# Kernel optimization log

Hardware: AMD Instinct MI355X
Metric: run time of the kernel (lower is better)

The kernel has to match this reference:

```python
import jax, jax.numpy as jnp
import numpy as np

B, S, N, IN_DIM = 64, 12, 170, 1
E, L, C, H, OUT = 128, 4, 2, 8, 1
OFFSET, PAD = 0, 1          # seq_offset=0 -> Conv2d padding (0,1)
LOOKUP, MAXLEN = 0, 100
EPS = 1e-5


def _shift(x, s):
    """y[:, i] = x[:, i+s] along axis 1, zero padded."""
    if s == 0:
        return x
    z = jnp.zeros_like(x[:, :abs(s)])
    if s > 0:
        return jnp.concatenate([x[:, s:], z], axis=1)
    return jnp.concatenate([z, x[:, :s]], axis=1)


def _masked_conv_diag(x, w):
    """Diagonal of Conv2d(kernel=(1,3), pad=(0,PAD)) applied to the causally
    masked repeated tensor, computed directly without the O(B*S*S*E) blowup:
      out[b,i] = sum_k W[:,:,k] @ (mask(i, i+k-PAD) * x[b, i+k-PAD])
    where mask(i,j) = (j <= i) or (j < OFFSET)."""
    i = jnp.arange(x.shape[1])
    out = None
    for k in range(3):
        s = k - PAD
        term = jnp.einsum('bse,oe->bso', _shift(x, s), w[:, :, k])
        if s > 0:  # only future taps can be masked out
            term = term * (i + s < OFFSET).astype(x.dtype)[None, :, None]
        out = term if out is None else out + term
    return out


def _conv1d_k3(x, w, b):
    """Conv1d over the seq dim, kernel 3, padding 1, with bias. x:[b,s,e]."""
    out = b
    for k in range(3):
        out = out + jnp.einsum('bse,oe->bso', _shift(x, k - 1), w[:, :, k])
    return out


def _layer_norm(x, g, b):
    m = jnp.mean(x, -1, keepdims=True)
    v = jnp.mean((x - m) ** 2, -1, keepdims=True)
    return (x - m) * jax.lax.rsqrt(v + EPS) * g + b


def _mha(q_in, kv_in, w, b, mask=None):
    dh = E // H
    q = (q_in @ w[0] + b[0]).reshape(q_in.shape[0], q_in.shape[1], H, dh)
    k = (kv_in @ w[1] + b[1]).reshape(kv_in.shape[0], kv_in.shape[1], H, dh)
    v = (kv_in @ w[2] + b[2]).reshape(kv_in.shape[0], kv_in.shape[1], H, dh)
    s = jnp.einsum('bqhd,bkhd->bhqk', q, k) * np.float32(1.0 / np.sqrt(dh))
    if mask is not None:
        s = jnp.where(mask[None, None], s, jnp.float32(-1e9))
    a = jax.nn.softmax(s, axis=-1)
    o = jnp.einsum('bhqk,bkhd->bqhd', a, v).reshape(q_in.shape[0], q_in.shape[1], E)
    return o @ w[3] + b[3]


def setup_inputs() -> dict:
    key = jax.random.key(0)
    ks = jax.random.split(key, 16)

    def nrm(k, shape, scale=0.05):
        return scale * jax.random.normal(k, shape, dtype=jnp.float32)

    # sinusoidal positional table, length MAXLEN
    pos = np.arange(MAXLEN)[:, None].astype(np.float32)
    div = np.exp(-np.log(10000.0) * np.arange(0, E, 2) / E).astype(np.float32)
    pe = np.zeros((MAXLEN, E), np.float32)
    pe[:, 0::2] = np.sin(pos * div)
    pe[:, 1::2] = np.cos(pos * div)

    return {
        'x': jax.random.normal(ks[0], (B, S, N, IN_DIM), jnp.float32),
        'enc_x': jax.random.normal(ks[1], (C, B * N, S, E), jnp.float32),
        'tgt_mask': jnp.tril(jnp.ones((S, S), bool)),
        'emb_w': nrm(ks[2], (IN_DIM, E), 1.0),
        'emb_b': jnp.zeros((E,), jnp.float32),
        'pe': jnp.asarray(pe),
        'conv_q_w': nrm(ks[3], (L, E, E, 3)),
        'conv_k_w': nrm(ks[4], (L, C, E, E, 3)),
        'conv_k_b': jnp.zeros((L, C, E), jnp.float32),
        'sa_w': nrm(ks[5], (L, 4, E, E)),
        'sa_b': jnp.zeros((L, 4, E), jnp.float32),
        'ca_w': nrm(ks[6], (L, C, 4, E, E)),
        'ca_b': jnp.zeros((L, C, 4, E), jnp.float32),
        'ff_w1': nrm(ks[7], (L, E, 4 * E)),
        'ff_b1': jnp.zeros((L, 4 * E), jnp.float32),
        'ff_w2': nrm(ks[8], (L, 4 * E, E)),
        'ff_b2': jnp.zeros((L, E), jnp.float32),
        'ln_g': jnp.ones((L, 3, E), jnp.float32),
        'ln_b': jnp.zeros((L, 3, E), jnp.float32),
        'fc_w': nrm(ks[9], (E, OUT)),
        'fc_b': jnp.zeros((OUT,), jnp.float32),
    }


def reference(x, enc_x, tgt_mask, emb_w, emb_b, pe, conv_q_w, conv_k_w, conv_k_b,
              sa_w, sa_b, ca_w, ca_b, ff_w1, ff_b1, ff_w2, ff_b2, ln_g, ln_b,
              fc_w, fc_b):
    h = x @ emb_w + emb_b                                    # [B,S,N,E]
    h = jnp.transpose(h, (1, 0, 2, 3)).reshape(S, B * N, E)  # [S,B*N,E]
    h = jnp.transpose(h, (1, 0, 2))                          # [B*N,S,E]
    h = h + pe[LOOKUP:LOOKUP + S]
    for l in range(L):
        # local trends: causal masked-conv query (the fused diagonal)
        h = _masked_conv_diag(h, conv_q_w[l])
        enc_list = [_conv1d_k3(enc_x[i], conv_k_w[l, i], conv_k_b[l, i])
                    for i in range(C)]
        # decoder block: self-attn -> cross-attn (avg over features) -> FFN
        h = _layer_norm(h + _mha(h, h, sa_w[l], sa_b[l], tgt_mask),
                        ln_g[l, 0], ln_b[l, 0])
        cross = sum(_mha(h, enc_list[i], ca_w[l, i], ca_b[l, i])
                    for i in range(C)) / C
        h = _layer_norm(h + cross, ln_g[l, 1], ln_b[l, 1])
        f = jax.nn.relu(h @ ff_w1[l] + ff_b1[l]) @ ff_w2[l] + ff_b2[l]
        h = _layer_norm(h + f, ln_g[l, 2], ln_b[l, 2])
    out = h @ fc_w + fc_b                                    # [B*N,S,OUT]
    out = jnp.transpose(out, (1, 0, 2)).reshape(S, B, N, OUT)
    return jnp.transpose(out, (1, 0, 2, 3))                  # [B,S,N,OUT]
```

## Files before the change

kernel.cpp:

```cpp
#include <hip/hip_runtime.h>


#define B_   64
#define S_   12
#define N_   170
#define BN_  (B_*N_)
#define E_   128
#define L_   4
#define C_   2
#define H_   8
#define DH_  16
#define FF_  512
#define EPS_ 1e-5f
#define THREADS 512

typedef unsigned short u16;
typedef __attribute__((ext_vector_type(4))) float f32x4;
typedef __attribute__((ext_vector_type(8))) u16   us8;
typedef __attribute__((ext_vector_type(4))) u16   us4;
typedef __attribute__((ext_vector_type(8))) __bf16 bf16x8;
union FragU { us8 u; bf16x8 b; };

__device__ __forceinline__ u16 f2bf(float f) {
    __bf16 h = (__bf16)f;
    return __builtin_bit_cast(u16, h);
}
__device__ __forceinline__ float bf2f(u16 s) {
    return __builtin_bit_cast(float, (unsigned)s << 16);
}

__global__ void k_wpack(const float* __restrict__ cq, const float* __restrict__ sa,
                        const float* __restrict__ ck, const float* __restrict__ ca,
                        const float* __restrict__ f1, const float* __restrict__ f2,
                        u16* __restrict__ wp) {
    int f  = blockIdx.x * 256 + threadIdx.x;
    int l  = f / 57344, fl = f % 57344;
    const float* src; int sk, so, KS, q;
    if (fl < 4096)        { int tap = fl >> 11; q = fl & 2047; KS = 4;
                            src = cq + (size_t)l*49152 + tap;            sk = 3;   so = 384; }
    else if (fl < 12288)  { int j = (fl - 4096) >> 11; q = fl & 2047; KS = 4;
                            src = sa + (size_t)(l*4 + j)*16384;          sk = 128; so = 1;   }
    else if (fl < 24576)  { int ct = (fl - 12288) >> 11; q = fl & 2047; KS = 4;
                            int ci = ct / 3, tap = ct % 3;
                            src = ck + (size_t)(l*2 + ci)*49152 + tap;   sk = 3;   so = 384; }
    else if (fl < 40960)  { int cj = (fl - 24576) >> 11; q = fl & 2047; KS = 4;
                            src = ca + (size_t)(l*8 + cj)*16384;         sk = 128; so = 1;   }
    else if (fl < 49152)  { q = fl - 40960; KS = 4;
                            src = f1 + (size_t)l*65536;                  sk = 512; so = 1;   }
    else                  { q = fl - 49152; KS = 16;
                            src = f2 + (size_t)l*65536;                  sk = 128; so = 1;   }
    int lane = q & 63, tt = q >> 6;
    int ks = tt % KS, ntile = tt / KS;
    int k0 = ks*32 + ((lane >> 4) << 3);
    int o  = ntile*16 + (lane & 15);
    us8 w;
    #pragma unroll
    for (int i = 0; i < 8; i++) w[i] = f2bf(src[(size_t)(k0 + i)*sk + (size_t)o*so]);
    *(us8*)(wp + (size_t)f*8) = w;
}

__device__ __forceinline__ void stage48(const float* __restrict__ src, u16* dst, int t) {
    for (int i = t; i < 1536; i += THREADS) {
        const f32x4 v = ((const f32x4*)src)[i];
        int elem = i << 2;
        int row = elem >> 7, colb = (elem & 127) << 1;
        us4 w; w[0] = f2bf(v[0]); w[1] = f2bf(v[1]); w[2] = f2bf(v[2]); w[3] = f2bf(v[3]);
        *(us4*)((char*)dst + (((row << 8) + colb) ^ ((row & 7) << 4))) = w;
    }
}

__device__ __forceinline__ void stage48_embed(const float* __restrict__ x,
    const float* __restrict__ ew, const float* __restrict__ eb,
    const float* __restrict__ pe, int bn0, u16* dst, int t) {
    for (int i = t; i < 1536; i += THREADS) {
        int elem = i << 2;
        int row = elem >> 7, col = elem & 127;
        int g = row / 12, s = row - g*12;
        int bn = bn0 + g, b = bn / N_, n = bn - b*N_;
        float xv = x[(b*S_ + s)*N_ + n];
        const f32x4 w  = *(const f32x4*)(ew + col);
        const f32x4 bb = *(const f32x4*)(eb + col);
        const f32x4 p  = *(const f32x4*)(pe + s*E_ + col);
        us4 o; o[0] = f2bf(xv*w[0] + bb[0] + p[0]); o[1] = f2bf(xv*w[1] + bb[1] + p[1]);
               o[2] = f2bf(xv*w[2] + bb[2] + p[2]); o[3] = f2bf(xv*w[3] + bb[3] + p[3]);
        *(us4*)((char*)dst + (((row << 8) + (col << 1)) ^ ((row & 7) << 4))) = o;
    }
}

__device__ __forceinline__ void acc_init(f32x4 (&acc)[3], const float* bias, int wave, int lane) {
    float bv = bias ? bias[wave*16 + (lane & 15)] : 0.f;
    #pragma unroll
    for (int mt = 0; mt < 3; mt++) {
        acc[mt][0] = bv; acc[mt][1] = bv; acc[mt][2] = bv; acc[mt][3] = bv;
    }
}

template<int KSTOT>
__device__ __forceinline__ void gemm48(const u16* A, const us8* __restrict__ WP, int ksOff,
                                       f32x4 (&acc)[3], int wave, int lane) {
    #pragma unroll
    for (int ks = 0; ks < 4; ks++) {
        bf16x8 a[3];
        #pragma unroll
        for (int mt = 0; mt < 3; mt++) {
            int row  = mt*16 + (lane & 15);
            int colb = (ks*32 + ((lane >> 4) << 3)) << 1;
            FragU fu; fu.u = *(const us8*)((const char*)A + (((row << 8) + colb) ^ ((row & 7) << 4)));
            a[mt] = fu.b;
        }
        FragU fb; fb.u = WP[(wave*KSTOT + ksOff + ks)*64 + lane];
        #pragma unroll
        for (int mt = 0; mt < 3; mt++)
            acc[mt] = __builtin_amdgcn_mfma_f32_16x16x32_bf16(a[mt], fb.b, acc[mt], 0, 0, 0);
    }
}

__device__ __forceinline__ void gemm48_rows(const u16* A, const u16* ZR, const int (&sr)[3],
                                            const us8* __restrict__ WP,
                                            f32x4 (&acc)[3], int wave, int lane) {
    #pragma unroll
    for (int ks = 0; ks < 4; ks++) {
        bf16x8 a[3];
        #pragma unroll
        for (int mt = 0; mt < 3; mt++) {
            int colb = (ks*32 + ((lane >> 4) << 3)) << 1;
            const char* p = (sr[mt] >= 0)
                ? (const char*)A + (((sr[mt] << 8) + colb) ^ ((sr[mt] & 7) << 4))
                : (const char*)ZR + colb;
            FragU fu; fu.u = *(const us8*)p;
            a[mt] = fu.b;
        }
        FragU fb; fb.u = WP[(wave*4 + ks)*64 + lane];
        #pragma unroll
        for (int mt = 0; mt < 3; mt++)
            acc[mt] = __builtin_amdgcn_mfma_f32_16x16x32_bf16(a[mt], fb.b, acc[mt], 0, 0, 0);
    }
}

template<bool RELU>
__device__ __forceinline__ void acc_store_bf(const f32x4 (&acc)[3], u16* Bp, int wave, int lane) {
    #pragma unroll
    for (int mt = 0; mt < 3; mt++)
    #pragma unroll
    for (int r = 0; r < 4; r++) {
        int row = mt*16 + ((lane >> 4) << 2) + r;
        int col = wave*16 + (lane & 15);
        float v = acc[mt][r];
        if (RELU) v = fmaxf(v, 0.f);
        *(u16*)((char*)Bp + (((row << 8) + (col << 1)) ^ ((row & 7) << 4))) = f2bf(v);
    }
}

__device__ __forceinline__ void ld16(const u16* Bf, int row, int colb, float* o16) {
    int x = (row & 7) << 4;
    int base = (row << 8) + colb;
    us8 u0 = *(const us8*)((const char*)Bf + (base ^ x));
    us8 u1 = *(const us8*)((const char*)Bf + ((base + 16) ^ x));
    #pragma unroll
    for (int d = 0; d < 8; d++) { o16[d] = bf2f(u0[d]); o16[8+d] = bf2f(u1[d]); }
}

template<bool MASK>
__device__ __forceinline__ void attn48(u16* QA, const u16* KB, const u16* VB, int t) {
    if (t < 384) {
        int g = t / 96, rem = t % 96;
        int hh = rem / 12, qi = rem % 12;
        int hb2 = hh << 5;
        int rq = g*12 + qi;
        float qv[16]; ld16(QA, rq, hb2, qv);
        float sc[12]; float mx = -1e30f;
        #pragma unroll
        for (int j = 0; j < 12; j++) {
            float kv[16]; ld16(KB, g*12 + j, hb2, kv);
            float s = 0.f;
            #pragma unroll
            for (int d = 0; d < 16; d++) s += qv[d]*kv[d];
            s *= 0.25f;
            if (MASK && j > qi) s = -1e30f;
            sc[j] = s; mx = fmaxf(mx, s);
        }
        float sum = 0.f;
        #pragma unroll
        for (int j = 0; j < 12; j++) { sc[j] = __expf(sc[j] - mx); sum += sc[j]; }
        float inv = 1.f/sum;
        float ov[16];
        #pragma unroll
        for (int d = 0; d < 16; d++) ov[d] = 0.f;
        #pragma unroll
        for (int j = 0; j < 12; j++) {
            float vv[16]; ld16(VB, g*12 + j, hb2, vv);
            #pragma unroll
            for (int d = 0; d < 16; d++) ov[d] += sc[j]*vv[d];
        }
        int x = (rq & 7) << 4;
        us8 w0, w1;
        #pragma unroll
        for (int d = 0; d < 8; d++) { w0[d] = f2bf(ov[d]*inv); w1[d] = f2bf(ov[8+d]*inv); }
        *(us8*)((char*)QA + (((rq << 8) + hb2) ^ x))      = w0;
        *(us8*)((char*)QA + (((rq << 8) + hb2 + 16) ^ x)) = w1;
    }
}

__device__ __forceinline__ void ln_inreg(f32x4 (&v)[3], float* lnbuf,
                                         const float* __restrict__ g, const float* __restrict__ bb,
                                         int wave, int lane) {
    int col = wave*16 + (lane & 15);
    float gc = g[col], bc = bb[col];
    #pragma unroll
    for (int mt = 0; mt < 3; mt++)
    #pragma unroll
    for (int r = 0; r < 4; r++) {
        float a = v[mt][r];
        float p = a, q = a*a;
        #pragma unroll
        for (int off = 1; off < 16; off <<= 1) { p += __shfl_xor(p, off); q += __shfl_xor(q, off); }
        if ((lane & 15) == 0) {
            int row = mt*16 + ((lane >> 4) << 2) + r;
            lnbuf[(row*8 + wave)*2]     = p;
            lnbuf[(row*8 + wave)*2 + 1] = q;
        }
    }
    __syncthreads();
    #pragma unroll
    for (int mt = 0; mt < 3; mt++)
    #pragma unroll
    for (int r = 0; r < 4; r++) {
        int row = mt*16 + ((lane >> 4) << 2) + r;
        float sum = 0.f, ss = 0.f;
        #pragma unroll
        for (int w2 = 0; w2 < 8; w2++) { sum += lnbuf[(row*8 + w2)*2]; ss += lnbuf[(row*8 + w2)*2 + 1]; }
        float m   = sum * (1.f/128.f);
        float var = ss * (1.f/128.f) - m*m;
        float inv = rsqrtf(var + EPS_);
        v[mt][r] = (v[mt][r] - m)*inv*gc + bc;
    }
}

template<bool EMB, bool FIN>
__global__ void __launch_bounds__(THREADS, 2)
k_layer(float* __restrict__ h, const float* __restrict__ x,
        const float* __restrict__ ew, const float* __restrict__ ebp, const float* __restrict__ pe,
        const float* __restrict__ encx, const u16* __restrict__ lw,
        const float* __restrict__ sab, const float* __restrict__ ckb, const float* __restrict__ cab,
        const float* __restrict__ fb1, const float* __restrict__ fb2,
        const float* __restrict__ lg, const float* __restrict__ lb,
        const float* __restrict__ fcw, const float* __restrict__ fcb,
        float* __restrict__ outp) {
    __shared__ __align__(16) u16 P0[6144], P1[6144], P2[6144], P3[6144], P4[6144], ZR[128];
    __shared__ __align__(16) float lnbuf[48*8*2];

    int t = threadIdx.x, wave = t >> 6, lane = t & 63;
    int bid = blockIdx.x;
    float* hp = h + (size_t)bid * (48*128);

    if (t < 64) ((unsigned*)ZR)[t] = 0;
    if (EMB) stage48_embed(x, ew, ebp, pe, bid*4, P0, t);
    else     stage48(hp, P0, t);
    __syncthreads();

    int gg[3], rr[3];
    #pragma unroll
    for (int mt = 0; mt < 3; mt++) { int m = mt*16 + (lane & 15); gg[mt] = m/12; rr[mt] = m - gg[mt]*12; }

    f32x4 cacc[3];
    acc_init(cacc, nullptr, wave, lane);
    {
        int sr[3];
        #pragma unroll
        for (int mt = 0; mt < 3; mt++) { int r2 = rr[mt] - 1; sr[mt] = (r2 >= 0) ? gg[mt]*12 + r2 : -1; }
        gemm48_rows(P0, ZR, sr, (const us8*)lw, cacc, wave, lane);
        #pragma unroll
        for (int mt = 0; mt < 3; mt++) sr[mt] = gg[mt]*12 + rr[mt];
        gemm48_rows(P0, ZR, sr, (const us8*)(lw + 16384), cacc, wave, lane);
    }
    acc_store_bf<false>(cacc, P1, wave, lane);
    __syncthreads();

    {
        const us8* sap = (const us8*)(lw + 32768);
        f32x4 a[3];
        acc_init(a, sab, wave, lane);        gemm48<4>(P1, sap,        0, a, wave, lane); acc_store_bf<false>(a, P0, wave, lane);
        acc_init(a, sab + 128, wave, lane);  gemm48<4>(P1, sap + 2048, 0, a, wave, lane); acc_store_bf<false>(a, P2, wave, lane);
        acc_init(a, sab + 256, wave, lane);  gemm48<4>(P1, sap + 4096, 0, a, wave, lane); acc_store_bf<false>(a, P3, wave, lane);
    }
    __syncthreads();
    attn48<true>(P0, P2, P3, t);
    __syncthreads();

    f32x4 hres[3];
    stage48(encx + (size_t)(bid*4) * (S_*E_), P2, t);
    {
        f32x4 a[3];
        acc_init(a, sab + 384, wave, lane);
        gemm48<4>(P0, (const us8*)(lw + 81920), 0, a, wave, lane);
        #pragma unroll
        for (int mt = 0; mt < 3; mt++) hres[mt] = a[mt] + cacc[mt];
    }
    ln_inreg(hres, lnbuf, lg, lb, wave, lane);
    acc_store_bf<false>(hres, P1, wave, lane);
    __syncthreads();

    f32x4 creg[3];
    {
        int col = wave*16 + (lane & 15);
        float bv = cab[3*128 + col] + cab[7*128 + col];
        #pragma unroll
        for (int mt = 0; mt < 3; mt++) { creg[mt][0]=bv; creg[mt][1]=bv; creg[mt][2]=bv; creg[mt][3]=bv; }
    }

    #pragma unroll
    for (int ci = 0; ci < 2; ci++) {
        {
            f32x4 a[3];
            acc_init(a, ckb + ci*128, wave, lane);
            #pragma unroll
            for (int tap = 0; tap < 3; tap++) {
                int sr[3];
                #pragma unroll
                for (int mt = 0; mt < 3; mt++) {
                    int r2 = rr[mt] + tap - 1;
                    sr[mt] = (r2 >= 0 && r2 < 12) ? gg[mt]*12 + r2 : -1;
                }
                gemm48_rows(P2, ZR, sr, (const us8*)(lw + 98304 + (ci*3 + tap)*16384), a, wave, lane);
            }
            acc_store_bf<false>(a, P3, wave, lane);
        }
        __syncthreads();
        const us8* cap = (const us8*)(lw + 196608 + ci*4*16384);
        {
            f32x4 a[3];
            acc_init(a, cab + (ci*4 + 0)*128, wave, lane); gemm48<4>(P1, cap,        0, a, wave, lane); acc_store_bf<false>(a, P0, wave, lane);
            acc_init(a, cab + (ci*4 + 1)*128, wave, lane); gemm48<4>(P3, cap + 2048, 0, a, wave, lane); acc_store_bf<false>(a, P2, wave, lane);
            acc_init(a, cab + (ci*4 + 2)*128, wave, lane); gemm48<4>(P3, cap + 4096, 0, a, wave, lane); acc_store_bf<false>(a, P4, wave, lane);
        }
        __syncthreads();
        attn48<false>(P0, P2, P4, t);
        __syncthreads();
        if (ci == 0) stage48(encx + ((size_t)BN_ + bid*4) * (S_*E_), P2, t);
        gemm48<4>(P0, cap + 6144, 0, creg, wave, lane);
        if (ci == 0) __syncthreads();
    }
    #pragma unroll
    for (int mt = 0; mt < 3; mt++) hres[mt] = hres[mt] + 0.5f*creg[mt];
    __syncthreads();
    ln_inreg(hres, lnbuf, lg + 128, lb + 128, wave, lane);
    acc_store_bf<false>(hres, P1, wave, lane);
    __syncthreads();

    f32x4 ffacc[3];
    acc_init(ffacc, fb2, wave, lane);
    #pragma unroll
    for (int c = 0; c < 4; c++) {
        u16* MB = (c & 1) ? P3 : P2;
        {
            f32x4 a[3];
            acc_init(a, fb1 + c*128, wave, lane);
            gemm48<4>(P1, (const us8*)(lw + 327680) + c*2048, 0, a, wave, lane);
            acc_store_bf<true>(a, MB, wave, lane);
        }
        __syncthreads();
        gemm48<16>(MB, (const us8*)(lw + 393216), c*4, ffacc, wave, lane);
    }
    #pragma unroll
    for (int mt = 0; mt < 3; mt++) hres[mt] = hres[mt] + ffacc[mt];
    ln_inreg(hres, lnbuf, lg + 256, lb + 256, wave, lane);

    if (FIN) {
        float fw = fcw[wave*16 + (lane & 15)];
        float pr[3][4];
        #pragma unroll
        for (int mt = 0; mt < 3; mt++)
        #pragma unroll
        for (int r = 0; r < 4; r++) {
            float p = hres[mt][r]*fw;
            #pragma unroll
            for (int off = 1; off < 16; off <<= 1) p += __shfl_xor(p, off);
            pr[mt][r] = p;
        }
        __syncthreads();
        if ((lane & 15) == 0) {
            #pragma unroll
            for (int mt = 0; mt < 3; mt++)
            #pragma unroll
            for (int r = 0; r < 4; r++) {
                int row = mt*16 + ((lane >> 4) << 2) + r;
                lnbuf[row*8 + wave] = pr[mt][r];
            }
        }
        __syncthreads();
        if (t < 48) {
            float s8 = fcb[0];
            #pragma unroll
            for (int w2 = 0; w2 < 8; w2++) s8 += lnbuf[t*8 + w2];
            int bn = bid*4 + t/12, s = t % 12;
            int b = bn / N_, n = bn - b*N_;
            outp[(b*S_ + s)*N_ + n] = s8;
        }
    } else {
        #pragma unroll
        for (int mt = 0; mt < 3; mt++)
        #pragma unroll
        for (int r = 0; r < 4; r++) {
            int row = mt*16 + ((lane >> 4) << 2) + r;
            int col = wave*16 + (lane & 15);
            hp[row*128 + col] = hres[mt][r];
        }
    }
}

extern "C" void kernel_launch(void* const* d_in, const int* in_sizes, int n_in,
                              void* d_out, int out_size, void* d_ws, size_t ws_size,
                              hipStream_t stream) {
    const float* x        = (const float*)d_in[0];
    const float* enc_x    = (const float*)d_in[1];
    const float* emb_w    = (const float*)d_in[3];
    const float* emb_b    = (const float*)d_in[4];
    const float* pe       = (const float*)d_in[5];
    const float* conv_q_w = (const float*)d_in[6];
    const float* conv_k_w = (const float*)d_in[7];
    const float* conv_k_b = (const float*)d_in[8];
    const float* sa_w     = (const float*)d_in[9];
    const float* sa_b     = (const float*)d_in[10];
    const float* ca_w     = (const float*)d_in[11];
    const float* ca_b     = (const float*)d_in[12];
    const float* ff_w1    = (const float*)d_in[13];
    const float* ff_b1    = (const float*)d_in[14];
    const float* ff_w2    = (const float*)d_in[15];
    const float* ff_b2    = (const float*)d_in[16];
    const float* ln_g     = (const float*)d_in[17];
    const float* ln_b     = (const float*)d_in[18];
    const float* fc_w     = (const float*)d_in[19];
    const float* fc_b     = (const float*)d_in[20];

    const size_t HN = (size_t)BN_ * S_ * E_;
    float* h  = (float*)d_ws;
    u16* wpk  = (u16*)((float*)d_ws + HN);

    k_wpack<<<896, 256, 0, stream>>>(conv_q_w, sa_w, conv_k_w, ca_w, ff_w1, ff_w2, wpk);

    for (int l = 0; l < L_; l++) {
        const u16* lw = wpk + (size_t)l*458752;
        const float* sab = sa_b + l*512;
        const float* ckb = conv_k_b + l*256;
        const float* cab = ca_b + l*1024;
        const float* fb1 = ff_b1 + l*512;
        const float* fb2 = ff_b2 + l*128;
        const float* lg  = ln_g + l*384;
        const float* lb  = ln_b + l*384;
        if (l == 0)
            k_layer<true, false><<<BN_/4, THREADS, 0, stream>>>(h, x, emb_w, emb_b, pe, enc_x, lw,
                sab, ckb, cab, fb1, fb2, lg, lb, fc_w, fc_b, (float*)d_out);
        else if (l == L_-1)
            k_layer<false, true><<<BN_/4, THREADS, 0, stream>>>(h, x, emb_w, emb_b, pe, enc_x, lw,
                sab, ckb, cab, fb1, fb2, lg, lb, fc_w, fc_b, (float*)d_out);
        else
            k_layer<false, false><<<BN_/4, THREADS, 0, stream>>>(h, x, emb_w, emb_b, pe, enc_x, lw,
                sab, ckb, cab, fb1, fb2, lg, lb, fc_w, fc_b, (float*)d_out);
    }
}
```

Before: 1.809 ms.

## Share A fragments across Q/K/V GEMMs and reschedule encoder staging loads

Adds multi-output GEMM helpers that load each A fragment from shared memory once and feed it to two or three weight matrices. The self-attention QKV and cross-attention K/V projections use them, which cuts LDS reads and gives more independent MFMAs per load. The first encoder tile is now staged into a free buffer at kernel start. The second is staged during the first cross-attention, and the per-channel loop is unrolled with rotated buffers. The cost is higher register pressure from three live accumulator sets, which may reduce occupancy.

```diff
diff --git a/kernel.cpp b/kernel.cpp
--- a/kernel.cpp
+++ b/kernel.cpp
@@ -95,23 +95,65 @@
     }
 }
 
+__device__ __forceinline__ bf16x8 ldA(const u16* A, int row, int colb) {
+    FragU fu; fu.u = *(const us8*)((const char*)A + (((row << 8) + colb) ^ ((row & 7) << 4)));
+    return fu.b;
+}
+
 template<int KSTOT>
 __device__ __forceinline__ void gemm48(const u16* A, const us8* __restrict__ WP, int ksOff,
                                        f32x4 (&acc)[3], int wave, int lane) {
     #pragma unroll
     for (int ks = 0; ks < 4; ks++) {
+        int colb = (ks*32 + ((lane >> 4) << 3)) << 1;
         bf16x8 a[3];
         #pragma unroll
-        for (int mt = 0; mt < 3; mt++) {
-            int row  = mt*16 + (lane & 15);
-            int colb = (ks*32 + ((lane >> 4) << 3)) << 1;
-            FragU fu; fu.u = *(const us8*)((const char*)A + (((row << 8) + colb) ^ ((row & 7) << 4)));
-            a[mt] = fu.b;
-        }
+        for (int mt = 0; mt < 3; mt++) a[mt] = ldA(A, mt*16 + (lane & 15), colb);
         FragU fb; fb.u = WP[(wave*KSTOT + ksOff + ks)*64 + lane];
         #pragma unroll
         for (int mt = 0; mt < 3; mt++)
             acc[mt] = __builtin_amdgcn_mfma_f32_16x16x32_bf16(a[mt], fb.b, acc[mt], 0, 0, 0);
+    }
+}
+
+__device__ __forceinline__ void gemm48_x3(const u16* A,
+        const us8* __restrict__ B0, const us8* __restrict__ B1, const us8* __restrict__ B2,
+        f32x4 (&c0)[3], f32x4 (&c1)[3], f32x4 (&c2)[3], int wave, int lane) {
+    #pragma unroll
+    for (int ks = 0; ks < 4; ks++) {
+        int colb = (ks*32 + ((lane >> 4) << 3)) << 1;
+        bf16x8 a[3];
+        #pragma unroll
+        for (int mt = 0; mt < 3; mt++) a[mt] = ldA(A, mt*16 + (lane & 15), colb);
+        FragU f0, f1, f2;
+        int bi = (wave*4 + ks)*64 + lane;
+        f0.u = B0[bi]; f1.u = B1[bi]; f2.u = B2[bi];
+        #pragma unroll
+        for (int mt = 0; mt < 3; mt++) {
+            c0[mt] = __builtin_amdgcn_mfma_f32_16x16x32_bf16(a[mt], f0.b, c0[mt], 0, 0, 0);
+            c1[mt] = __builtin_amdgcn_mfma_f32_16x16x32_bf16(a[mt], f1.b, c1[mt], 0, 0, 0);
+            c2[mt] = __builtin_amdgcn_mfma_f32_16x16x32_bf16(a[mt], f2.b, c2[mt], 0, 0, 0);
+        }
+    }
+}
+
+__device__ __forceinline__ void gemm48_x2(const u16* A,
+        const us8* __restrict__ B0, const us8* __restrict__ B1,
+        f32x4 (&c0)[3], f32x4 (&c1)[3], int wave, int lane) {
+    #pragma unroll
+    for (int ks = 0; ks < 4; ks++) {
+        int colb = (ks*32 + ((lane >> 4) << 3)) << 1;
+        bf16x8 a[3];
+        #pragma unroll
+        for (int mt = 0; mt < 3; mt++) a[mt] = ldA(A, mt*16 + (lane & 15), colb);
+        FragU f0, f1;
+        int bi = (wave*4 + ks)*64 + lane;
+        f0.u = B0[bi]; f1.u = B1[bi];
+        #pragma unroll
+        for (int mt = 0; mt < 3; mt++) {
+            c0[mt] = __builtin_amdgcn_mfma_f32_16x16x32_bf16(a[mt], f0.b, c0[mt], 0, 0, 0);
+            c1[mt] = __builtin_amdgcn_mfma_f32_16x16x32_bf16(a[mt], f1.b, c1[mt], 0, 0, 0);
+        }
     }
 }
 
@@ -120,10 +162,10 @@
                                             f32x4 (&acc)[3], int wave, int lane) {
     #pragma unroll
     for (int ks = 0; ks < 4; ks++) {
+        int colb = (ks*32 + ((lane >> 4) << 3)) << 1;
         bf16x8 a[3];
         #pragma unroll
         for (int mt = 0; mt < 3; mt++) {
-            int colb = (ks*32 + ((lane >> 4) << 3)) << 1;
             const char* p = (sr[mt] >= 0)
                 ? (const char*)A + (((sr[mt] << 8) + colb) ^ ((sr[mt] & 7) << 4))
                 : (const char*)ZR + colb;
@@ -256,6 +298,7 @@
     if (t < 64) ((unsigned*)ZR)[t] = 0;
     if (EMB) stage48_embed(x, ew, ebp, pe, bid*4, P0, t);
     else     stage48(hp, P0, t);
+    stage48(encx + (size_t)(bid*4) * (S_*E_), P4, t);
     __syncthreads();
 
     int gg[3], rr[3];
@@ -278,17 +321,20 @@
 
     {
         const us8* sap = (const us8*)(lw + 32768);
-        f32x4 a[3];
-        acc_init(a, sab, wave, lane);        gemm48<4>(P1, sap,        0, a, wave, lane); acc_store_bf<false>(a, P0, wave, lane);
-        acc_init(a, sab + 128, wave, lane);  gemm48<4>(P1, sap + 2048, 0, a, wave, lane); acc_store_bf<false>(a, P2, wave, lane);
-        acc_init(a, sab + 256, wave, lane);  gemm48<4>(P1, sap + 4096, 0, a, wave, lane); acc_store_bf<false>(a, P3, wave, lane);
+        f32x4 aq[3], ak[3], av[3];
+        acc_init(aq, sab,       wave, lane);
+        acc_init(ak, sab + 128, wave, lane);
+        acc_init(av, sab + 256, wave, lane);
+        gemm48_x3(P1, sap, sap + 2048, sap + 4096, aq, ak, av, wave, lane);
+        acc_store_bf<false>(aq, P0, wave, lane);
+        acc_store_bf<false>(ak, P2, wave, lane);
+        acc_store_bf<false>(av, P3, wave, lane);
     }
     __syncthreads();
     attn48<true>(P0, P2, P3, t);
     __syncthreads();
 
     f32x4 hres[3];
-    stage48(encx + (size_t)(bid*4) * (S_*E_), P2, t);
     {
         f32x4 a[3];
         acc_init(a, sab + 384, wave, lane);
@@ -307,39 +353,70 @@
         #pragma unroll
         for (int mt = 0; mt < 3; mt++) { creg[mt][0]=bv; creg[mt][1]=bv; creg[mt][2]=bv; creg[mt][3]=bv; }
     }
-
-    #pragma unroll
-    for (int ci = 0; ci < 2; ci++) {
-        {
-            f32x4 a[3];
-            acc_init(a, ckb + ci*128, wave, lane);
-            #pragma unroll
-            for (int tap = 0; tap < 3; tap++) {
-                int sr[3];
-                #pragma unroll
-                for (int mt = 0; mt < 3; mt++) {
-                    int r2 = rr[mt] + tap - 1;
-                    sr[mt] = (r2 >= 0 && r2 < 12) ? gg[mt]*12 + r2 : -1;
-                }
-                gemm48_rows(P2, ZR, sr, (const us8*)(lw + 98304 + (ci*3 + tap)*16384), a, wave, lane);
-            }
-            acc_store_bf<false>(a, P3, wave, lane);
-        }
-        __syncthreads();
-        const us8* cap = (const us8*)(lw + 196608 + ci*4*16384);
-        {
-            f32x4 a[3];
-            acc_init(a, cab + (ci*4 + 0)*128, wave, lane); gemm48<4>(P1, cap,        0, a, wave, lane); acc_store_bf<false>(a, P0, wave, lane);
-            acc_init(a, cab + (ci*4 + 1)*128, wave, lane); gemm48<4>(P3, cap + 2048, 0, a, wave, lane); acc_store_bf<false>(a, P2, wave, lane);
-            acc_init(a, cab + (ci*4 + 2)*128, wave, lane); gemm48<4>(P3, cap + 4096, 0, a, wave, lane); acc_store_bf<false>(a, P4, wave, lane);
-        }
-        __syncthreads();
-        attn48<false>(P0, P2, P4, t);
-        __syncthreads();
-        if (ci == 0) stage48(encx + ((size_t)BN_ + bid*4) * (S_*E_), P2, t);
-        gemm48<4>(P0, cap + 6144, 0, creg, wave, lane);
-        if (ci == 0) __syncthreads();
-    }
+    int srf[3], srp[3], srn[3];
+    #pragma unroll
+    for (int mt = 0; mt < 3; mt++) {
+        int r2 = rr[mt] - 1; srp[mt] = (r2 >= 0) ? gg[mt]*12 + r2 : -1;
+        srf[mt] = gg[mt]*12 + rr[mt];
+        r2 = rr[mt] + 1;     srn[mt] = (r2 < 12) ? gg[mt]*12 + r2 : -1;
+    }
+
+    {
+        const us8* ckp = (const us8*)(lw + 98304);
+        f32x4 a[3];
+        acc_init(a, ckb, wave, lane);
+        gemm48_rows(P4, ZR, srp, ckp,        a, wave, lane);
+        gemm48_rows(P4, ZR, srf, ckp + 2048, a, wave, lane);
+        gemm48_rows(P4, ZR, srn, ckp + 4096, a, wave, lane);
+        acc_store_bf<false>(a, P3, wave, lane);
+    }
+    __syncthreads();
+    const us8* cap0 = (const us8*)(lw + 196608);
+    {
+        f32x4 aq[3], ak[3], av[3];
+        acc_init(aq, cab,           wave, lane);
+        gemm48<4>(P1, cap0, 0, aq, wave, lane);
+        acc_store_bf<false>(aq, P0, wave, lane);
+        acc_init(ak, cab + 128, wave, lane);
+        acc_init(av, cab + 256, wave, lane);
+        gemm48_x2(P3, cap0 + 2048, cap0 + 4096, ak, av, wave, lane);
+        acc_store_bf<false>(ak, P2, wave, lane);
+        acc_store_bf<false>(av, P4, wave, lane);
+    }
+    __syncthreads();
+    stage48(encx + ((size_t)BN_ + bid*4) * (S_*E_), P3, t);
+    attn48<false>(P0, P2, P4, t);
+    __syncthreads();
+    gemm48<4>(P0, cap0 + 6144, 0, creg, wave, lane);
+    __syncthreads();
+
+    {
+        const us8* ckp = (const us8*)(lw + 98304 + 3*16384);
+        f32x4 a[3];
+        acc_init(a, ckb + 128, wave, lane);
+        gemm48_rows(P3, ZR, srp, ckp,        a, wave, lane);
+        gemm48_rows(P3, ZR, srf, ckp + 2048, a, wave, lane);
+        gemm48_rows(P3, ZR, srn, ckp + 4096, a, wave, lane);
+        acc_store_bf<false>(a, P0, wave, lane);
+    }
+    __syncthreads();
+    const us8* cap1 = (const us8*)(lw + 196608 + 4*16384);
+    {
+        f32x4 aq[3], ak[3], av[3];
+        acc_init(aq, cab + 4*128, wave, lane);
+        gemm48<4>(P1, cap1, 0, aq, wave, lane);
+        acc_store_bf<false>(aq, P2, wave, lane);
+        acc_init(ak, cab + 5*128, wave, lane);
+        acc_init(av, cab + 6*128, wave, lane);
+        gemm48_x2(P0, cap1 + 2048, cap1 + 4096, ak, av, wave, lane);
+        acc_store_bf<false>(ak, P3, wave, lane);
+        acc_store_bf<false>(av, P4, wave, lane);
+    }
+    __syncthreads();
+    attn48<false>(P2, P3, P4, t);
+    __syncthreads();
+    gemm48<4>(P2, cap1 + 6144, 0, creg, wave, lane);
+
     #pragma unroll
     for (int mt = 0; mt < 3; mt++) hres[mt] = hres[mt] + 0.5f*creg[mt];
     __syncthreads();
```

New measurement: 1.832 ms. About the same (+1.3%).
